# Performance work log

Hardware: AMD Instinct MI355X
Metric: run time of the kernel (lower is better)

Reference implementation:

```python
import math
import jax
import jax.numpy as jnp
import numpy as np

N_IMG = 8
A = 3
H = 100
W = 100
STRIDE = 16
IMG = 1600
PRE_NMS_TOP_N = 2000
POST_NMS_TOP_N = 1000
NMS_THRESH = 0.7
MIN_SIZE = 0
BBOX_XFORM_CLIP = math.log(1000.0 / 16.0)


def setup_inputs() -> dict:
    key = jax.random.key(0)
    k1, k2 = jax.random.split(key)
    objectness = jax.random.normal(k1, (N_IMG, A, H, W), jnp.float32)
    box_regression = jax.random.normal(k2, (N_IMG, A * 4, H, W), jnp.float32) * 0.5
    # Grid anchors, flattened in (H, W, A) order to match objectness.permute(0,2,3,1)
    cy = (jnp.arange(H, dtype=jnp.float32) + 0.5) * STRIDE  # [H]
    cx = (jnp.arange(W, dtype=jnp.float32) + 0.5) * STRIDE  # [W]
    half = jnp.array([64.0, 128.0, 256.0], jnp.float32) / 2.0  # [A]
    cy = cy[:, None, None]  # [H,1,1]
    cx = cx[None, :, None]  # [1,W,1]
    s = half[None, None, :]  # [1,1,A]
    x1, y1, x2, y2 = jnp.broadcast_arrays(cx - s, cy - s, cx + s, cy + s)
    anc = jnp.stack([x1, y1, x2, y2], axis=-1).reshape(-1, 4)  # [H*W*A, 4]
    anchors = jnp.broadcast_to(anc[None], (N_IMG, H * W * A, 4)).copy()
    return {
        "objectness": objectness,
        "box_regression": box_regression,
        "anchors": anchors,
        "image_height": IMG,
        "image_width": IMG,
    }


def _decode(deltas, boxes):
    # BoxCoder(weights=(1,1,1,1)).decode with TO_REMOVE=1
    widths = boxes[..., 2] - boxes[..., 0] + 1.0
    heights = boxes[..., 3] - boxes[..., 1] + 1.0
    ctr_x = boxes[..., 0] + 0.5 * widths
    ctr_y = boxes[..., 1] + 0.5 * heights
    dx, dy = deltas[..., 0], deltas[..., 1]
    dw = jnp.minimum(deltas[..., 2], BBOX_XFORM_CLIP)
    dh = jnp.minimum(deltas[..., 3], BBOX_XFORM_CLIP)
    pcx = dx * widths + ctr_x
    pcy = dy * heights + ctr_y
    pw = jnp.exp(dw) * widths
    ph = jnp.exp(dh) * heights
    return jnp.stack(
        [pcx - 0.5 * pw, pcy - 0.5 * ph, pcx + 0.5 * pw - 1.0, pcy + 0.5 * ph - 1.0],
        axis=-1,
    )


def _nms_keep(boxes, valid, thresh):
    # boxes [n,4] sorted by descending score; valid: pre-filter mask.
    n = boxes.shape[0]
    x1, y1, x2, y2 = boxes[:, 0], boxes[:, 1], boxes[:, 2], boxes[:, 3]
    areas = (x2 - x1 + 1.0) * (y2 - y1 + 1.0)
    xx1 = jnp.maximum(x1[:, None], x1[None, :])
    yy1 = jnp.maximum(y1[:, None], y1[None, :])
    xx2 = jnp.minimum(x2[:, None], x2[None, :])
    yy2 = jnp.minimum(y2[:, None], y2[None, :])
    inter = jnp.maximum(xx2 - xx1 + 1.0, 0.0) * jnp.maximum(yy2 - yy1 + 1.0, 0.0)
    iou = inter / (areas[:, None] + areas[None, :] - inter)
    idx = jnp.arange(n)

    def body(i, keep):
        sup = keep[i] & (iou[i] > thresh) & (idx > i)
        return keep & ~sup

    return jax.lax.fori_loop(0, n, body, valid)


def _forward(objectness, box_regression, anchors, image_height, image_width):
    N, A_, H_, W_ = objectness.shape
    scores = jax.nn.sigmoid(objectness.transpose(0, 2, 3, 1).reshape(N, -1))  # [N, A*H*W]
    deltas = (
        box_regression.reshape(N, A_, 4, H_, W_)
        .transpose(0, 3, 4, 1, 2)
        .reshape(N, -1, 4)
    )
    pre = min(PRE_NMS_TOP_N, scores.shape[1])
    top_scores, top_idx = jax.lax.top_k(scores, pre)  # sorted descending
    deltas = jnp.take_along_axis(deltas, top_idx[:, :, None], axis=1)
    anc = jnp.take_along_axis(anchors, top_idx[:, :, None], axis=1)
    props = _decode(deltas, anc)  # [N, pre, 4]
    # clip to image (fact = 1)
    xs = jnp.clip(props[..., 0::2], 0.0, image_width - 1.0)
    ys = jnp.clip(props[..., 1::2], 0.0, image_height - 1.0)
    props = jnp.stack([xs[..., 0], ys[..., 0], xs[..., 1], ys[..., 1]], axis=-1)
    # filter small / out-of-image-center boxes
    ws = props[..., 2] - props[..., 0] + 1.0
    hs = props[..., 3] - props[..., 1] + 1.0
    xc = props[..., 0] + ws / 2.0
    yc = props[..., 1] + hs / 2.0
    valid = (ws >= MIN_SIZE) & (hs >= MIN_SIZE) & (xc < image_width) & (yc < image_height)
    keep = jax.vmap(lambda b, v: _nms_keep(b, v, NMS_THRESH))(props, valid)

    def _select(b, s, k):
        # compact kept boxes (already score-sorted) into fixed-size output
        rank = jnp.cumsum(k) - 1
        tgt = jnp.where(k & (rank < POST_NMS_TOP_N), rank, POST_NMS_TOP_N)
        ob = jnp.zeros((POST_NMS_TOP_N + 1, 4), b.dtype).at[tgt].set(b)[:POST_NMS_TOP_N]
        os = jnp.zeros((POST_NMS_TOP_N + 1,), s.dtype).at[tgt].set(s)[:POST_NMS_TOP_N]
        ov = jnp.arange(POST_NMS_TOP_N) < jnp.minimum(jnp.sum(k), POST_NMS_TOP_N)
        return ob, os, ov

    return jax.vmap(_select)(props, top_scores, keep)


def reference(objectness, box_regression, anchors, image_height, image_width):
    # Returns (boxes [N,post,4], objectness scores [N,post], valid mask [N,post])
    return _forward(objectness, box_regression, anchors, image_height, image_width)
```

## Files before the change

### kernel.cpp

```cpp
#include <hip/hip_runtime.h>
#include <math.h>
#include <stdint.h>

#define NIMG   8
#define NA     30000
#define PRE_N  2000
#define POST_N 1000
#define NMS_TH 0.7f
#define DCLIP  4.135166556742356f
#define IMGF   1600.0f
#define IMGM1  1599.0f
#define CAND_MAX 4096


__global__ __launch_bounds__(1024) void hist_compact(
    const float* __restrict__ obj,
    uint64_t* __restrict__ candBuf, unsigned int* __restrict__ candCnt)
{
    const int n    = blockIdx.x;
    const int tid  = threadIdx.x;
    const int lane = tid & 63;
    const int wid  = tid >> 6;

    __shared__ unsigned int hist[4096];
    __shared__ unsigned int wsum[16];
    __shared__ unsigned int scal[4];

    for (int b = tid; b < 4096; b += 1024) hist[b] = 0u;
    if (tid < 4) scal[tid] = 0u;
    __syncthreads();

    const float* objn = obj + n * NA;

    for (int j = tid; j < NA; j += 1024) {
        unsigned int u = __float_as_uint(objn[j]);
        unsigned int k = (u & 0x80000000u) ? ~u : (u | 0x80000000u);
        atomicAdd(&hist[k >> 20], 1u);
    }
    __syncthreads();

    unsigned int c0 = hist[tid*4+0], c1 = hist[tid*4+1],
                 c2 = hist[tid*4+2], c3 = hist[tid*4+3];
    unsigned int p = c0 + c1 + c2 + c3;
    unsigned int s = p;
    #pragma unroll
    for (int off = 1; off < 64; off <<= 1) {
        unsigned int v = __shfl_down(s, off);
        if (lane + off < 64) s += v;
    }
    if (lane == 0) wsum[wid] = s;
    __syncthreads();
    unsigned int wafter = 0;
    for (int w = wid + 1; w < 16; ++w) wafter += wsum[w];
    unsigned int after = (s - p) + wafter;
    {
        unsigned int S3 = after + c3;
        unsigned int S2 = S3 + c2;
        unsigned int S1 = S2 + c1;
        unsigned int S0 = S1 + c0;
        if (S3 >= PRE_N && after < PRE_N) { scal[2] = tid*4+3; }
        if (S2 >= PRE_N && S3    < PRE_N) { scal[2] = tid*4+2; }
        if (S1 >= PRE_N && S2    < PRE_N) { scal[2] = tid*4+1; }
        if (S0 >= PRE_N && S1    < PRE_N) { scal[2] = tid*4+0; }
    }
    __syncthreads();
    const unsigned int bstar = scal[2];

    for (int j = tid; j < NA; j += 1024) {
        unsigned int u = __float_as_uint(objn[j]);
        unsigned int k = (u & 0x80000000u) ? ~u : (u | 0x80000000u);
        if ((k >> 20) < bstar) continue;
        int a = j / 10000, t = j - a * 10000;
        uint64_t key = (((uint64_t)(~k)) << 32) | (unsigned int)(t * 3 + a);
        unsigned int pos = atomicAdd(&scal[0], 1u);
        if (pos < CAND_MAX) candBuf[n * CAND_MAX + pos] = key;
    }
    __syncthreads();
    if (tid == 0) candCnt[n] = min(scal[0], (unsigned int)CAND_MAX);
}

__global__ __launch_bounds__(64) void rank_decode(
    const float* __restrict__ breg,
    const uint64_t* __restrict__ candBuf, const unsigned int* __restrict__ candCnt,
    float* __restrict__ wsBoxes, float* __restrict__ wsScores,
    int* __restrict__ wsValid)
{
    const int n    = blockIdx.x >> 6;
    const int tile = blockIdx.x & 63;
    const int lane = threadIdx.x;

    const int C = (int)candCnt[n];
    if (tile * 64 >= C) return;

    const uint64_t* cb = candBuf + n * CAND_MAX;
    const int my = tile * 64 + lane;
    const uint64_t km = (my < C) ? cb[my] : ~0ull;

    unsigned int rank = 0;
    const int nch = (C + 63) >> 6;
    for (int ch = 0; ch < nch; ++ch) {
        const int j = ch * 64 + lane;
        uint64_t ck = (j < C) ? cb[j] : ~0ull;
        unsigned int clo = (unsigned int)ck, chi = (unsigned int)(ck >> 32);
        #pragma unroll
        for (int c = 0; c < 64; ++c) {
            unsigned int lo = (unsigned int)__builtin_amdgcn_readlane((int)clo, c);
            unsigned int hi = (unsigned int)__builtin_amdgcn_readlane((int)chi, c);
            uint64_t kc = ((uint64_t)hi << 32) | lo;
            rank += (kc < km) ? 1u : 0u;
        }
    }
    if (my >= C || rank >= PRE_N) return;

    unsigned int idx = (unsigned int)km;
    unsigned int k   = ~((unsigned int)(km >> 32));
    unsigned int u   = (k & 0x80000000u) ? (k & 0x7fffffffu) : ~k;
    float logit = __uint_as_float(u);
    float score = 1.0f / (1.0f + expf(-logit));

    int a = idx % 3, t = idx / 3, w = t % 100, h = t / 100;
    const float* bp = breg + n*120000 + (a*4)*10000 + t;
    float dx = bp[0], dy = bp[10000], dw = bp[20000], dh = bp[30000];

    float half = (a == 0) ? 32.0f : ((a == 1) ? 64.0f : 128.0f);
    float cx = w * 16.0f + 8.0f, cy = h * 16.0f + 8.0f;
    float x1 = cx - half, y1 = cy - half, x2 = cx + half, y2 = cy + half;
    float wd = x2 - x1 + 1.0f, hg = y2 - y1 + 1.0f;
    float cxr = x1 + 0.5f * wd, cyr = y1 + 0.5f * hg;
    dw = fminf(dw, DCLIP); dh = fminf(dh, DCLIP);
    float pcx = dx * wd + cxr, pcy = dy * hg + cyr;
    float pw = expf(dw) * wd, ph = expf(dh) * hg;
    float px1 = pcx - 0.5f * pw, py1 = pcy - 0.5f * ph;
    float px2 = pcx + 0.5f * pw - 1.0f, py2 = pcy + 0.5f * ph - 1.0f;
    px1 = fminf(fmaxf(px1, 0.0f), IMGM1);
    px2 = fminf(fmaxf(px2, 0.0f), IMGM1);
    py1 = fminf(fmaxf(py1, 0.0f), IMGM1);
    py2 = fminf(fmaxf(py2, 0.0f), IMGM1);
    float wss = px2 - px1 + 1.0f, hss = py2 - py1 + 1.0f;
    float xc = px1 + wss * 0.5f, yc = py1 + hss * 0.5f;
    int valid = (wss >= 0.0f) && (hss >= 0.0f) && (xc < IMGF) && (yc < IMGF);

    ((float4*)wsBoxes)[n * PRE_N + (int)rank] = make_float4(px1, py1, px2, py2);
    wsScores[n * PRE_N + (int)rank] = score;
    wsValid [n * PRE_N + (int)rank] = valid;
}

__global__ __launch_bounds__(512) void nms_mask(
    const float* __restrict__ wsBoxes, uint64_t* __restrict__ mask)
{
    const int blk  = blockIdx.x;
    const int n    = blk >> 5;
    const int i_t  = blk & 31;
    const int tid  = threadIdx.x;
    const int lane = tid & 63;
    const int wv   = tid >> 6;

    __shared__ uint64_t tile[64 * 33];

    for (int idx = tid; idx < 64 * 33; idx += 512) tile[idx] = 0ull;
    __syncthreads();

    const int r = i_t * 64 + lane;
    float4 rb = (r < PRE_N) ? ((const float4*)wsBoxes)[n * PRE_N + r]
                            : make_float4(0.f, 0.f, 0.f, 0.f);
    float ra = (rb.z - rb.x + 1.0f) * (rb.w - rb.y + 1.0f);

    for (int j_t = i_t + wv; j_t < 32; j_t += 8) {
        const int j = j_t * 64 + lane;
        float4 cb = (j < PRE_N) ? ((const float4*)wsBoxes)[n * PRE_N + j]
                                : make_float4(3e30f, 3e30f, 3e30f, 3e30f);
        float ca = (cb.z - cb.x + 1.0f) * (cb.w - cb.y + 1.0f);
        const uint64_t jmask = (j_t == 31) ? 0xFFFFull : ~0ull;
        const bool diag = (j_t == i_t);
        uint64_t myword = 0ull;

        #pragma unroll
        for (int c = 0; c < 64; ++c) {
            float rx1 = __int_as_float(__builtin_amdgcn_readlane(__float_as_int(rb.x), c));
            float ry1 = __int_as_float(__builtin_amdgcn_readlane(__float_as_int(rb.y), c));
            float rx2 = __int_as_float(__builtin_amdgcn_readlane(__float_as_int(rb.z), c));
            float ry2 = __int_as_float(__builtin_amdgcn_readlane(__float_as_int(rb.w), c));
            float rar = __int_as_float(__builtin_amdgcn_readlane(__float_as_int(ra), c));
            float xx1 = fmaxf(rx1, cb.x), yy1 = fmaxf(ry1, cb.y);
            float xx2 = fminf(rx2, cb.z), yy2 = fminf(ry2, cb.w);
            float ww = fmaxf(xx2 - xx1 + 1.0f, 0.0f);
            float hh = fmaxf(yy2 - yy1 + 1.0f, 0.0f);
            float inter = ww * hh;
            float denom = rar + ca - inter;
            unsigned long long bits = __ballot(inter > NMS_TH * denom) & jmask;
            if (diag) bits &= (c == 63) ? 0ull : ((~0ull) << (c + 1));
            if (lane == c) myword = bits;
        }
        tile[lane * 33 + j_t] = myword;
    }
    __syncthreads();

    uint64_t* mrow = mask + ((size_t)n * PRE_N + (size_t)i_t * 64) * 32;
    const int cmax = (i_t == 31) ? 16 : 64;
    for (int idx = tid; idx < cmax * 32; idx += 512) {
        const int rr = idx >> 5, w = idx & 31;
        mrow[idx] = tile[rr * 33 + w];
    }
}

#define SL(n,b) \
    "global_load_dword v" #n ", %[voff], %[sbase]\n\t" \
    "v_add_u32 %[voff], 0x100, %[voff]\n\t"

#define SS(n,b) \
    "s_waitcnt vmcnt(63)\n\t" \
    "v_readlane_b32 %[t], v" #n ", %[lw]\n\t" \
    "s_bitcmp1_b32 %[win], " #b "\n\t" \
    "s_cselect_b32 %[m], 0, -1\n\t" \
    "s_sub_i32 %[kept], %[kept], %[m]\n\t" \
    "s_and_b32 %[t], %[t], %[m]\n\t" \
    "s_or_b32 %[win], %[win], %[t]\n\t" \
    "v_and_b32 v" #n ", %[m], v" #n "\n\t" \
    "v_or_b32 %[rem], %[rem], v" #n "\n\t" \
    "global_load_dword v" #n ", %[voff], %[sbase]\n\t" \
    "v_add_u32 %[voff], 0x100, %[voff]\n\t"

#define SN(n,b,w) \
    "s_waitcnt vmcnt(" #w ")\n\t" \
    "v_readlane_b32 %[t], v" #n ", %[lw]\n\t" \
    "s_bitcmp1_b32 %[win], " #b "\n\t" \
    "s_cselect_b32 %[m], 0, -1\n\t" \
    "s_sub_i32 %[kept], %[kept], %[m]\n\t" \
    "s_and_b32 %[t], %[t], %[m]\n\t" \
    "s_or_b32 %[win], %[win], %[t]\n\t" \
    "v_and_b32 v" #n ", %[m], v" #n "\n\t" \
    "v_or_b32 %[rem], %[rem], v" #n "\n\t"

#define SWIN \
    "s_add_u32 %[lw], %[lw], 1\n\t" \
    "v_readlane_b32 %[t], %[rem], %[lw]\n\t" \
    "s_mov_b32 %[win], %[t]\n\t"

#define ROW_A(M) M(64,0) M(65,1) M(66,2) M(67,3) M(68,4) M(69,5) M(70,6) M(71,7) \
    M(72,8) M(73,9) M(74,10) M(75,11) M(76,12) M(77,13) M(78,14) M(79,15) \
    M(80,16) M(81,17) M(82,18) M(83,19) M(84,20) M(85,21) M(86,22) M(87,23) \
    M(88,24) M(89,25) M(90,26) M(91,27) M(92,28) M(93,29) M(94,30) M(95,31)
#define ROW_B(M) M(96,0) M(97,1) M(98,2) M(99,3) M(100,4) M(101,5) M(102,6) M(103,7) \
    M(104,8) M(105,9) M(106,10) M(107,11) M(108,12) M(109,13) M(110,14) M(111,15) \
    M(112,16) M(113,17) M(114,18) M(115,19) M(116,20) M(117,21) M(118,22) M(119,23) \
    M(120,24) M(121,25) M(122,26) M(123,27) M(124,28) M(125,29) M(126,30) M(127,31)

__global__ __launch_bounds__(256) void nms_scan_select(
    const float* __restrict__ wsBoxes, const float* __restrict__ wsScores,
    const int* __restrict__ wsValid, const uint64_t* __restrict__ mask,
    float* __restrict__ out)
{
    const int n   = blockIdx.x;
    const int tid = threadIdx.x;

    __shared__ __align__(8) unsigned char invb[256];
    __shared__ unsigned int keepw32[64];
    __shared__ int sscan[256];

    unsigned int byte = 0xFFu;
    if (tid < PRE_N / 8) {
        byte = 0u;
        for (int q = 0; q < 8; ++q)
            byte |= (wsValid[n * PRE_N + tid * 8 + q] ? 0u : 1u) << q;
    }
    invb[tid] = (unsigned char)byte;
    __syncthreads();

    if (tid < 64) {
        unsigned int rem = ((const unsigned int*)invb)[tid];
        unsigned long long sbase =
            (unsigned long long)(const void*)(mask + (size_t)n * PRE_N * 32);
        unsigned int voff = (unsigned int)(tid * 4);
        int win_, m_, t_, lw_, kept_, cnt_;

        asm volatile(
            "s_waitcnt vmcnt(0) lgkmcnt(0)\n\t"
            "s_mov_b32 %[kept], 0\n\t"
            "s_mov_b32 %[lw], 0\n\t"
            ROW_A(SL) ROW_B(SL)
            "v_readlane_b32 %[t], %[rem], %[lw]\n\t"
            "s_mov_b32 %[win], %[t]\n\t"
            "s_mov_b32 %[cnt], 30\n\t"
            "Lnms_%=:\n\t"
            ROW_A(SS)
            SWIN
            ROW_B(SS)
            SWIN
            "s_cmp_ge_i32 %[kept], 0x3e8\n\t"
            "s_cbranch_scc1 Lend_%=\n\t"
            "s_sub_u32 %[cnt], %[cnt], 1\n\t"
            "s_cmp_lg_u32 %[cnt], 0\n\t"
            "s_cbranch_scc1 Lnms_%=\n\t"
            SS(64,0) SS(65,1) SS(66,2) SS(67,3) SS(68,4) SS(69,5) SS(70,6) SS(71,7)
            SS(72,8) SS(73,9) SS(74,10) SS(75,11) SS(76,12) SS(77,13) SS(78,14) SS(79,15)
            SN(80,16,63) SN(81,17,62) SN(82,18,61) SN(83,19,60)
            SN(84,20,59) SN(85,21,58) SN(86,22,57) SN(87,23,56)
            SN(88,24,55) SN(89,25,54) SN(90,26,53) SN(91,27,52)
            SN(92,28,51) SN(93,29,50) SN(94,30,49) SN(95,31,48)
            SWIN
            SN(96,0,47) SN(97,1,46) SN(98,2,45) SN(99,3,44)
            SN(100,4,43) SN(101,5,42) SN(102,6,41) SN(103,7,40)
            SN(104,8,39) SN(105,9,38) SN(106,10,37) SN(107,11,36)
            SN(108,12,35) SN(109,13,34) SN(110,14,33) SN(111,15,32)
            SN(112,16,31) SN(113,17,30) SN(114,18,29) SN(115,19,28)
            SN(116,20,27) SN(117,21,26) SN(118,22,25) SN(119,23,24)
            SN(120,24,23) SN(121,25,22) SN(122,26,21) SN(123,27,20)
            SN(124,28,19) SN(125,29,18) SN(126,30,17) SN(127,31,16)
            SWIN
            SN(64,0,15) SN(65,1,14) SN(66,2,13) SN(67,3,12)
            SN(68,4,11) SN(69,5,10) SN(70,6,9) SN(71,7,8)
            SN(72,8,7) SN(73,9,6) SN(74,10,5) SN(75,11,4)
            SN(76,12,3) SN(77,13,2) SN(78,14,1) SN(79,15,0)
            "Lend_%=:\n\t"
            "s_waitcnt vmcnt(0)\n\t"
            : [rem]"+v"(rem), [voff]"+v"(voff),
              [win]"=&s"(win_), [m]"=&s"(m_), [t]"=&s"(t_),
              [lw]"=&s"(lw_), [kept]"=&s"(kept_), [cnt]"=&s"(cnt_)
            : [sbase]"s"(sbase)
            : "scc", "vcc", "memory",
              "v64","v65","v66","v67","v68","v69","v70","v71",
              "v72","v73","v74","v75","v76","v77","v78","v79",
              "v80","v81","v82","v83","v84","v85","v86","v87",
              "v88","v89","v90","v91","v92","v93","v94","v95",
              "v96","v97","v98","v99","v100","v101","v102","v103",
              "v104","v105","v106","v107","v108","v109","v110","v111",
              "v112","v113","v114","v115","v116","v117","v118","v119",
              "v120","v121","v122","v123","v124","v125","v126","v127");

        keepw32[tid] = ~rem;
    }
    __syncthreads();

    int c[8]; const int base8 = tid * 8;
    int lsum = 0;
    for (int q = 0; q < 8; ++q) {
        const int i = base8 + q;
        c[q] = (i < PRE_N) ? (int)((keepw32[i >> 5] >> (i & 31)) & 1u) : 0;
        lsum += c[q];
    }
    sscan[tid] = lsum;
    __syncthreads();
    for (int off = 1; off < 256; off <<= 1) {
        int v = (tid >= off) ? sscan[tid - off] : 0;
        __syncthreads();
        sscan[tid] += v;
        __syncthreads();
    }
    const int excl  = sscan[tid] - lsum;
    const int total = sscan[255];

    float* ob  = out + n * POST_N * 4;
    float* osc = out + NIMG * POST_N * 4 + n * POST_N;
    float* ovd = out + NIMG * POST_N * 5 + n * POST_N;

    for (int i = tid; i < POST_N * 4; i += 256) ob[i] = 0.0f;
    for (int i = tid; i < POST_N; i += 256) osc[i] = 0.0f;
    const int lim = min(total, POST_N);
    for (int i = tid; i < POST_N; i += 256) ovd[i] = (i < lim) ? 1.0f : 0.0f;
    __syncthreads();

    int run = excl;
    for (int q = 0; q < 8; ++q) {
        const int i = base8 + q;
        if (i < PRE_N && c[q]) {
            if (run < POST_N) {
                float4 b = ((const float4*)wsBoxes)[n * PRE_N + i];
                ob[run * 4 + 0] = b.x;
                ob[run * 4 + 1] = b.y;
                ob[run * 4 + 2] = b.z;
                ob[run * 4 + 3] = b.w;
                osc[run] = wsScores[n * PRE_N + i];
            }
            run++;
        }
    }
}

extern "C" void kernel_launch(void* const* d_in, const int* in_sizes, int n_in,
                              void* d_out, int out_size, void* d_ws, size_t ws_size,
                              hipStream_t stream) {
    const float* obj  = (const float*)d_in[0];
    const float* breg = (const float*)d_in[1];
    float* ws        = (float*)d_ws;
    float* wsBoxes   = ws;
    float* wsScores  = ws + 64000;
    int*   wsValid   = (int*)(ws + 80000);
    uint64_t* wsMask = (uint64_t*)(ws + 96000);
    uint64_t*     candBuf = wsMask;
    unsigned int* candCnt = (unsigned int*)(wsMask + NIMG * CAND_MAX);

    hist_compact<<<NIMG, 1024, 0, stream>>>(obj, candBuf, candCnt);
    rank_decode<<<NIMG * 64, 64, 0, stream>>>(breg, candBuf, candCnt,
                                              wsBoxes, wsScores, wsValid);
    nms_mask<<<NIMG * 32, 512, 0, stream>>>(wsBoxes, wsMask);
    nms_scan_select<<<NIMG, 256, 0, stream>>>(wsBoxes, wsScores, wsValid, wsMask,
                                              (float*)d_out);
}
```

Baseline: 184.1 us.

## Fuse RPN pipeline into one cooperative kernel with grid-wide syncs

```diff
diff --git a/kernel.cpp b/kernel.cpp
--- a/kernel.cpp
+++ b/kernel.cpp
@@ -1,6 +1,9 @@
 #include <hip/hip_runtime.h>
+#include <hip/hip_cooperative_groups.h>
 #include <math.h>
 #include <stdint.h>
+
+namespace cg = cooperative_groups;
 
 #define NIMG   8
 #define NA     30000
@@ -11,197 +14,8 @@
 #define IMGF   1600.0f
 #define IMGM1  1599.0f
 #define CAND_MAX 4096
-
-
-__global__ __launch_bounds__(1024) void hist_compact(
-    const float* __restrict__ obj,
-    uint64_t* __restrict__ candBuf, unsigned int* __restrict__ candCnt)
-{
-    const int n    = blockIdx.x;
-    const int tid  = threadIdx.x;
-    const int lane = tid & 63;
-    const int wid  = tid >> 6;
-
-    __shared__ unsigned int hist[4096];
-    __shared__ unsigned int wsum[16];
-    __shared__ unsigned int scal[4];
-
-    for (int b = tid; b < 4096; b += 1024) hist[b] = 0u;
-    if (tid < 4) scal[tid] = 0u;
-    __syncthreads();
-
-    const float* objn = obj + n * NA;
-
-    for (int j = tid; j < NA; j += 1024) {
-        unsigned int u = __float_as_uint(objn[j]);
-        unsigned int k = (u & 0x80000000u) ? ~u : (u | 0x80000000u);
-        atomicAdd(&hist[k >> 20], 1u);
-    }
-    __syncthreads();
-
-    unsigned int c0 = hist[tid*4+0], c1 = hist[tid*4+1],
-                 c2 = hist[tid*4+2], c3 = hist[tid*4+3];
-    unsigned int p = c0 + c1 + c2 + c3;
-    unsigned int s = p;
-    #pragma unroll
-    for (int off = 1; off < 64; off <<= 1) {
-        unsigned int v = __shfl_down(s, off);
-        if (lane + off < 64) s += v;
-    }
-    if (lane == 0) wsum[wid] = s;
-    __syncthreads();
-    unsigned int wafter = 0;
-    for (int w = wid + 1; w < 16; ++w) wafter += wsum[w];
-    unsigned int after = (s - p) + wafter;
-    {
-        unsigned int S3 = after + c3;
-        unsigned int S2 = S3 + c2;
-        unsigned int S1 = S2 + c1;
-        unsigned int S0 = S1 + c0;
-        if (S3 >= PRE_N && after < PRE_N) { scal[2] = tid*4+3; }
-        if (S2 >= PRE_N && S3    < PRE_N) { scal[2] = tid*4+2; }
-        if (S1 >= PRE_N && S2    < PRE_N) { scal[2] = tid*4+1; }
-        if (S0 >= PRE_N && S1    < PRE_N) { scal[2] = tid*4+0; }
-    }
-    __syncthreads();
-    const unsigned int bstar = scal[2];
-
-    for (int j = tid; j < NA; j += 1024) {
-        unsigned int u = __float_as_uint(objn[j]);
-        unsigned int k = (u & 0x80000000u) ? ~u : (u | 0x80000000u);
-        if ((k >> 20) < bstar) continue;
-        int a = j / 10000, t = j - a * 10000;
-        uint64_t key = (((uint64_t)(~k)) << 32) | (unsigned int)(t * 3 + a);
-        unsigned int pos = atomicAdd(&scal[0], 1u);
-        if (pos < CAND_MAX) candBuf[n * CAND_MAX + pos] = key;
-    }
-    __syncthreads();
-    if (tid == 0) candCnt[n] = min(scal[0], (unsigned int)CAND_MAX);
-}
-
-__global__ __launch_bounds__(64) void rank_decode(
-    const float* __restrict__ breg,
-    const uint64_t* __restrict__ candBuf, const unsigned int* __restrict__ candCnt,
-    float* __restrict__ wsBoxes, float* __restrict__ wsScores,
-    int* __restrict__ wsValid)
-{
-    const int n    = blockIdx.x >> 6;
-    const int tile = blockIdx.x & 63;
-    const int lane = threadIdx.x;
-
-    const int C = (int)candCnt[n];
-    if (tile * 64 >= C) return;
-
-    const uint64_t* cb = candBuf + n * CAND_MAX;
-    const int my = tile * 64 + lane;
-    const uint64_t km = (my < C) ? cb[my] : ~0ull;
-
-    unsigned int rank = 0;
-    const int nch = (C + 63) >> 6;
-    for (int ch = 0; ch < nch; ++ch) {
-        const int j = ch * 64 + lane;
-        uint64_t ck = (j < C) ? cb[j] : ~0ull;
-        unsigned int clo = (unsigned int)ck, chi = (unsigned int)(ck >> 32);
-        #pragma unroll
-        for (int c = 0; c < 64; ++c) {
-            unsigned int lo = (unsigned int)__builtin_amdgcn_readlane((int)clo, c);
-            unsigned int hi = (unsigned int)__builtin_amdgcn_readlane((int)chi, c);
-            uint64_t kc = ((uint64_t)hi << 32) | lo;
-            rank += (kc < km) ? 1u : 0u;
-        }
-    }
-    if (my >= C || rank >= PRE_N) return;
-
-    unsigned int idx = (unsigned int)km;
-    unsigned int k   = ~((unsigned int)(km >> 32));
-    unsigned int u   = (k & 0x80000000u) ? (k & 0x7fffffffu) : ~k;
-    float logit = __uint_as_float(u);
-    float score = 1.0f / (1.0f + expf(-logit));
-
-    int a = idx % 3, t = idx / 3, w = t % 100, h = t / 100;
-    const float* bp = breg + n*120000 + (a*4)*10000 + t;
-    float dx = bp[0], dy = bp[10000], dw = bp[20000], dh = bp[30000];
-
-    float half = (a == 0) ? 32.0f : ((a == 1) ? 64.0f : 128.0f);
-    float cx = w * 16.0f + 8.0f, cy = h * 16.0f + 8.0f;
-    float x1 = cx - half, y1 = cy - half, x2 = cx + half, y2 = cy + half;
-    float wd = x2 - x1 + 1.0f, hg = y2 - y1 + 1.0f;
-    float cxr = x1 + 0.5f * wd, cyr = y1 + 0.5f * hg;
-    dw = fminf(dw, DCLIP); dh = fminf(dh, DCLIP);
-    float pcx = dx * wd + cxr, pcy = dy * hg + cyr;
-    float pw = expf(dw) * wd, ph = expf(dh) * hg;
-    float px1 = pcx - 0.5f * pw, py1 = pcy - 0.5f * ph;
-    float px2 = pcx + 0.5f * pw - 1.0f, py2 = pcy + 0.5f * ph - 1.0f;
-    px1 = fminf(fmaxf(px1, 0.0f), IMGM1);
-    px2 = fminf(fmaxf(px2, 0.0f), IMGM1);
-    py1 = fminf(fmaxf(py1, 0.0f), IMGM1);
-    py2 = fminf(fmaxf(py2, 0.0f), IMGM1);
-    float wss = px2 - px1 + 1.0f, hss = py2 - py1 + 1.0f;
-    float xc = px1 + wss * 0.5f, yc = py1 + hss * 0.5f;
-    int valid = (wss >= 0.0f) && (hss >= 0.0f) && (xc < IMGF) && (yc < IMGF);
-
-    ((float4*)wsBoxes)[n * PRE_N + (int)rank] = make_float4(px1, py1, px2, py2);
-    wsScores[n * PRE_N + (int)rank] = score;
-    wsValid [n * PRE_N + (int)rank] = valid;
-}
-
-__global__ __launch_bounds__(512) void nms_mask(
-    const float* __restrict__ wsBoxes, uint64_t* __restrict__ mask)
-{
-    const int blk  = blockIdx.x;
-    const int n    = blk >> 5;
-    const int i_t  = blk & 31;
-    const int tid  = threadIdx.x;
-    const int lane = tid & 63;
-    const int wv   = tid >> 6;
-
-    __shared__ uint64_t tile[64 * 33];
-
-    for (int idx = tid; idx < 64 * 33; idx += 512) tile[idx] = 0ull;
-    __syncthreads();
-
-    const int r = i_t * 64 + lane;
-    float4 rb = (r < PRE_N) ? ((const float4*)wsBoxes)[n * PRE_N + r]
-                            : make_float4(0.f, 0.f, 0.f, 0.f);
-    float ra = (rb.z - rb.x + 1.0f) * (rb.w - rb.y + 1.0f);
-
-    for (int j_t = i_t + wv; j_t < 32; j_t += 8) {
-        const int j = j_t * 64 + lane;
-        float4 cb = (j < PRE_N) ? ((const float4*)wsBoxes)[n * PRE_N + j]
-                                : make_float4(3e30f, 3e30f, 3e30f, 3e30f);
-        float ca = (cb.z - cb.x + 1.0f) * (cb.w - cb.y + 1.0f);
-        const uint64_t jmask = (j_t == 31) ? 0xFFFFull : ~0ull;
-        const bool diag = (j_t == i_t);
-        uint64_t myword = 0ull;
-
-        #pragma unroll
-        for (int c = 0; c < 64; ++c) {
-            float rx1 = __int_as_float(__builtin_amdgcn_readlane(__float_as_int(rb.x), c));
-            float ry1 = __int_as_float(__builtin_amdgcn_readlane(__float_as_int(rb.y), c));
-            float rx2 = __int_as_float(__builtin_amdgcn_readlane(__float_as_int(rb.z), c));
-            float ry2 = __int_as_float(__builtin_amdgcn_readlane(__float_as_int(rb.w), c));
-            float rar = __int_as_float(__builtin_amdgcn_readlane(__float_as_int(ra), c));
-            float xx1 = fmaxf(rx1, cb.x), yy1 = fmaxf(ry1, cb.y);
-            float xx2 = fminf(rx2, cb.z), yy2 = fminf(ry2, cb.w);
-            float ww = fmaxf(xx2 - xx1 + 1.0f, 0.0f);
-            float hh = fmaxf(yy2 - yy1 + 1.0f, 0.0f);
-            float inter = ww * hh;
-            float denom = rar + ca - inter;
-            unsigned long long bits = __ballot(inter > NMS_TH * denom) & jmask;
-            if (diag) bits &= (c == 63) ? 0ull : ((~0ull) << (c + 1));
-            if (lane == c) myword = bits;
-        }
-        tile[lane * 33 + j_t] = myword;
-    }
-    __syncthreads();
-
-    uint64_t* mrow = mask + ((size_t)n * PRE_N + (size_t)i_t * 64) * 32;
-    const int cmax = (i_t == 31) ? 16 : 64;
-    for (int idx = tid; idx < cmax * 32; idx += 512) {
-        const int rr = idx >> 5, w = idx & 31;
-        mrow[idx] = tile[rr * 33 + w];
-    }
-}
+#define NBLK   256
+#define NTHR   512
 
 #define SL(n,b) \
     "global_load_dword v" #n ", %[voff], %[sbase]\n\t" \
@@ -245,133 +59,312 @@
     M(112,16) M(113,17) M(114,18) M(115,19) M(116,20) M(117,21) M(118,22) M(119,23) \
     M(120,24) M(121,25) M(122,26) M(123,27) M(124,28) M(125,29) M(126,30) M(127,31)
 
-__global__ __launch_bounds__(256) void nms_scan_select(
-    const float* __restrict__ wsBoxes, const float* __restrict__ wsScores,
-    const int* __restrict__ wsValid, const uint64_t* __restrict__ mask,
+__global__ __launch_bounds__(NTHR) void rpn_mega(
+    const float* __restrict__ obj, const float* __restrict__ breg,
+    float* __restrict__ wsBoxes, float* __restrict__ wsScores,
+    int* __restrict__ wsValid, uint64_t* __restrict__ candBuf,
+    unsigned int* __restrict__ candCnt, unsigned int* __restrict__ bstarArr,
+    unsigned int* __restrict__ gHist, uint64_t* __restrict__ mask,
     float* __restrict__ out)
 {
-    const int n   = blockIdx.x;
-    const int tid = threadIdx.x;
-
-    __shared__ __align__(8) unsigned char invb[256];
-    __shared__ unsigned int keepw32[64];
-    __shared__ int sscan[256];
-
-    unsigned int byte = 0xFFu;
-    if (tid < PRE_N / 8) {
-        byte = 0u;
-        for (int q = 0; q < 8; ++q)
-            byte |= (wsValid[n * PRE_N + tid * 8 + q] ? 0u : 1u) << q;
-    }
-    invb[tid] = (unsigned char)byte;
-    __syncthreads();
-
-    if (tid < 64) {
-        unsigned int rem = ((const unsigned int*)invb)[tid];
-        unsigned long long sbase =
-            (unsigned long long)(const void*)(mask + (size_t)n * PRE_N * 32);
-        unsigned int voff = (unsigned int)(tid * 4);
-        int win_, m_, t_, lw_, kept_, cnt_;
-
-        asm volatile(
-            "s_waitcnt vmcnt(0) lgkmcnt(0)\n\t"
-            "s_mov_b32 %[kept], 0\n\t"
-            "s_mov_b32 %[lw], 0\n\t"
-            ROW_A(SL) ROW_B(SL)
-            "v_readlane_b32 %[t], %[rem], %[lw]\n\t"
-            "s_mov_b32 %[win], %[t]\n\t"
-            "s_mov_b32 %[cnt], 30\n\t"
-            "Lnms_%=:\n\t"
-            ROW_A(SS)
-            SWIN
-            ROW_B(SS)
-            SWIN
-            "s_cmp_ge_i32 %[kept], 0x3e8\n\t"
-            "s_cbranch_scc1 Lend_%=\n\t"
-            "s_sub_u32 %[cnt], %[cnt], 1\n\t"
-            "s_cmp_lg_u32 %[cnt], 0\n\t"
-            "s_cbranch_scc1 Lnms_%=\n\t"
-            SS(64,0) SS(65,1) SS(66,2) SS(67,3) SS(68,4) SS(69,5) SS(70,6) SS(71,7)
-            SS(72,8) SS(73,9) SS(74,10) SS(75,11) SS(76,12) SS(77,13) SS(78,14) SS(79,15)
-            SN(80,16,63) SN(81,17,62) SN(82,18,61) SN(83,19,60)
-            SN(84,20,59) SN(85,21,58) SN(86,22,57) SN(87,23,56)
-            SN(88,24,55) SN(89,25,54) SN(90,26,53) SN(91,27,52)
-            SN(92,28,51) SN(93,29,50) SN(94,30,49) SN(95,31,48)
-            SWIN
-            SN(96,0,47) SN(97,1,46) SN(98,2,45) SN(99,3,44)
-            SN(100,4,43) SN(101,5,42) SN(102,6,41) SN(103,7,40)
-            SN(104,8,39) SN(105,9,38) SN(106,10,37) SN(107,11,36)
-            SN(108,12,35) SN(109,13,34) SN(110,14,33) SN(111,15,32)
-            SN(112,16,31) SN(113,17,30) SN(114,18,29) SN(115,19,28)
-            SN(116,20,27) SN(117,21,26) SN(118,22,25) SN(119,23,24)
-            SN(120,24,23) SN(121,25,22) SN(122,26,21) SN(123,27,20)
-            SN(124,28,19) SN(125,29,18) SN(126,30,17) SN(127,31,16)
-            SWIN
-            SN(64,0,15) SN(65,1,14) SN(66,2,13) SN(67,3,12)
-            SN(68,4,11) SN(69,5,10) SN(70,6,9) SN(71,7,8)
-            SN(72,8,7) SN(73,9,6) SN(74,10,5) SN(75,11,4)
-            SN(76,12,3) SN(77,13,2) SN(78,14,1) SN(79,15,0)
-            "Lend_%=:\n\t"
-            "s_waitcnt vmcnt(0)\n\t"
-            : [rem]"+v"(rem), [voff]"+v"(voff),
-              [win]"=&s"(win_), [m]"=&s"(m_), [t]"=&s"(t_),
-              [lw]"=&s"(lw_), [kept]"=&s"(kept_), [cnt]"=&s"(cnt_)
-            : [sbase]"s"(sbase)
-            : "scc", "vcc", "memory",
-              "v64","v65","v66","v67","v68","v69","v70","v71",
-              "v72","v73","v74","v75","v76","v77","v78","v79",
-              "v80","v81","v82","v83","v84","v85","v86","v87",
-              "v88","v89","v90","v91","v92","v93","v94","v95",
-              "v96","v97","v98","v99","v100","v101","v102","v103",
-              "v104","v105","v106","v107","v108","v109","v110","v111",
-              "v112","v113","v114","v115","v116","v117","v118","v119",
-              "v120","v121","v122","v123","v124","v125","v126","v127");
-
-        keepw32[tid] = ~rem;
-    }
-    __syncthreads();
-
-    int c[8]; const int base8 = tid * 8;
-    int lsum = 0;
-    for (int q = 0; q < 8; ++q) {
-        const int i = base8 + q;
-        c[q] = (i < PRE_N) ? (int)((keepw32[i >> 5] >> (i & 31)) & 1u) : 0;
-        lsum += c[q];
-    }
-    sscan[tid] = lsum;
-    __syncthreads();
-    for (int off = 1; off < 256; off <<= 1) {
-        int v = (tid >= off) ? sscan[tid - off] : 0;
-        __syncthreads();
-        sscan[tid] += v;
-        __syncthreads();
-    }
-    const int excl  = sscan[tid] - lsum;
-    const int total = sscan[255];
-
-    float* ob  = out + n * POST_N * 4;
-    float* osc = out + NIMG * POST_N * 4 + n * POST_N;
-    float* ovd = out + NIMG * POST_N * 5 + n * POST_N;
-
-    for (int i = tid; i < POST_N * 4; i += 256) ob[i] = 0.0f;
-    for (int i = tid; i < POST_N; i += 256) osc[i] = 0.0f;
-    const int lim = min(total, POST_N);
-    for (int i = tid; i < POST_N; i += 256) ovd[i] = (i < lim) ? 1.0f : 0.0f;
-    __syncthreads();
-
-    int run = excl;
-    for (int q = 0; q < 8; ++q) {
-        const int i = base8 + q;
-        if (i < PRE_N && c[q]) {
-            if (run < POST_N) {
-                float4 b = ((const float4*)wsBoxes)[n * PRE_N + i];
-                ob[run * 4 + 0] = b.x;
-                ob[run * 4 + 1] = b.y;
-                ob[run * 4 + 2] = b.z;
-                ob[run * 4 + 3] = b.w;
-                osc[run] = wsScores[n * PRE_N + i];
+    cg::grid_group grid = cg::this_grid();
+    const int blk  = blockIdx.x;
+    const int tid  = threadIdx.x;
+    const int lane = tid & 63;
+    const int wid  = tid >> 6;
+    const int g    = blk * NTHR + tid;
+
+    __shared__ uint64_t sTile[64 * 33];
+    __shared__ int      sScan[NTHR];
+    __shared__ unsigned int sWsum[8];
+    __shared__ unsigned int sScal[4];
+    __shared__ __align__(8) unsigned char sInvb[256];
+    __shared__ unsigned int sKeep[64];
+
+    if (g < NIMG * 4096) gHist[g] = 0u;
+    if (g < NIMG) { candCnt[g] = 0u; bstarArr[g] = 0u; }
+    grid.sync();
+
+    for (int i = g; i < NIMG * NA; i += NBLK * NTHR) {
+        const int n = i / NA;
+        unsigned int u = __float_as_uint(obj[i]);
+        unsigned int k = (u & 0x80000000u) ? ~u : (u | 0x80000000u);
+        atomicAdd(&gHist[n * 4096 + (k >> 20)], 1u);
+    }
+    grid.sync();
+
+    if (blk < NIMG) {
+        const int n = blk;
+        unsigned int cb8[8], p = 0;
+        for (int q = 0; q < 8; ++q) { cb8[q] = gHist[n * 4096 + tid * 8 + q]; p += cb8[q]; }
+        unsigned int s = p;
+        #pragma unroll
+        for (int off = 1; off < 64; off <<= 1) {
+            unsigned int v = __shfl_down(s, off);
+            if (lane + off < 64) s += v;
+        }
+        if (lane == 0) sWsum[wid] = s;
+        __syncthreads();
+        unsigned int wafter = 0;
+        for (int w = wid + 1; w < 8; ++w) wafter += sWsum[w];
+        unsigned int suf = (s - p) + wafter;
+        for (int q = 7; q >= 0; --q) {
+            unsigned int Sq = suf + cb8[q];
+            if (Sq >= PRE_N && suf < PRE_N) sScal[0] = (unsigned int)(tid * 8 + q);
+            suf = Sq;
+        }
+        __syncthreads();
+        if (tid == 0) bstarArr[n] = sScal[0];
+    }
+    grid.sync();
+
+    for (int i = g; i < NIMG * NA; i += NBLK * NTHR) {
+        const int n = i / NA;
+        const int j = i - n * NA;
+        unsigned int u = __float_as_uint(obj[i]);
+        unsigned int k = (u & 0x80000000u) ? ~u : (u | 0x80000000u);
+        if ((k >> 20) >= bstarArr[n]) {
+            int a = j / 10000, t = j - a * 10000;
+            uint64_t key = (((uint64_t)(~k)) << 32) | (unsigned int)(t * 3 + a);
+            unsigned int pos = atomicAdd(&candCnt[n], 1u);
+            if (pos < CAND_MAX) candBuf[n * CAND_MAX + pos] = key;
+        }
+    }
+    grid.sync();
+
+    {
+        const int gw = blk * 8 + wid;
+        if (gw < NIMG * 64) {
+            const int n = gw >> 6, tile = gw & 63;
+            const int C = min((int)candCnt[n], CAND_MAX);
+            if (tile * 64 < C) {
+                const uint64_t* cb = candBuf + n * CAND_MAX;
+                const int my = tile * 64 + lane;
+                const uint64_t km = (my < C) ? cb[my] : ~0ull;
+                unsigned int rank = 0;
+                const int nch = (C + 63) >> 6;
+                for (int ch = 0; ch < nch; ++ch) {
+                    const int j = ch * 64 + lane;
+                    uint64_t ck = (j < C) ? cb[j] : ~0ull;
+                    unsigned int clo = (unsigned int)ck, chi = (unsigned int)(ck >> 32);
+                    #pragma unroll
+                    for (int c2 = 0; c2 < 64; ++c2) {
+                        unsigned int lo = (unsigned int)__builtin_amdgcn_readlane((int)clo, c2);
+                        unsigned int hi = (unsigned int)__builtin_amdgcn_readlane((int)chi, c2);
+                        uint64_t kc = ((uint64_t)hi << 32) | lo;
+                        rank += (kc < km) ? 1u : 0u;
+                    }
+                }
+                if (my < C && rank < PRE_N) {
+                    unsigned int idx = (unsigned int)km;
+                    unsigned int k   = ~((unsigned int)(km >> 32));
+                    unsigned int u   = (k & 0x80000000u) ? (k & 0x7fffffffu) : ~k;
+                    float logit = __uint_as_float(u);
+                    float score = 1.0f / (1.0f + expf(-logit));
+
+                    int a = idx % 3, t = idx / 3, w = t % 100, h = t / 100;
+                    const float* bp = breg + n*120000 + (a*4)*10000 + t;
+                    float dx = bp[0], dy = bp[10000], dw = bp[20000], dh = bp[30000];
+
+                    float half = (a == 0) ? 32.0f : ((a == 1) ? 64.0f : 128.0f);
+                    float cx = w * 16.0f + 8.0f, cy = h * 16.0f + 8.0f;
+                    float x1 = cx - half, y1 = cy - half, x2 = cx + half, y2 = cy + half;
+                    float wd = x2 - x1 + 1.0f, hg = y2 - y1 + 1.0f;
+                    float cxr = x1 + 0.5f * wd, cyr = y1 + 0.5f * hg;
+                    dw = fminf(dw, DCLIP); dh = fminf(dh, DCLIP);
+                    float pcx = dx * wd + cxr, pcy = dy * hg + cyr;
+                    float pw = expf(dw) * wd, ph = expf(dh) * hg;
+                    float px1 = pcx - 0.5f * pw, py1 = pcy - 0.5f * ph;
+                    float px2 = pcx + 0.5f * pw - 1.0f, py2 = pcy + 0.5f * ph - 1.0f;
+                    px1 = fminf(fmaxf(px1, 0.0f), IMGM1);
+                    px2 = fminf(fmaxf(px2, 0.0f), IMGM1);
+                    py1 = fminf(fmaxf(py1, 0.0f), IMGM1);
+                    py2 = fminf(fmaxf(py2, 0.0f), IMGM1);
+                    float wss = px2 - px1 + 1.0f, hss = py2 - py1 + 1.0f;
+                    float xc = px1 + wss * 0.5f, yc = py1 + hss * 0.5f;
+                    int valid = (wss >= 0.0f) && (hss >= 0.0f) && (xc < IMGF) && (yc < IMGF);
+
+                    ((float4*)wsBoxes)[n * PRE_N + (int)rank] = make_float4(px1, py1, px2, py2);
+                    wsScores[n * PRE_N + (int)rank] = score;
+                    wsValid [n * PRE_N + (int)rank] = valid;
+                }
             }
-            run++;
+        }
+    }
+    grid.sync();
+
+    {
+        const int n   = blk >> 5;
+        const int i_t = blk & 31;
+
+        for (int idx = tid; idx < 64 * 33; idx += NTHR) sTile[idx] = 0ull;
+        __syncthreads();
+
+        const int r = i_t * 64 + lane;
+        float4 rb = (r < PRE_N) ? ((const float4*)wsBoxes)[n * PRE_N + r]
+                                : make_float4(0.f, 0.f, 0.f, 0.f);
+        float ra = (rb.z - rb.x + 1.0f) * (rb.w - rb.y + 1.0f);
+
+        for (int j_t = i_t + wid; j_t < 32; j_t += 8) {
+            const int j = j_t * 64 + lane;
+            float4 cbx = (j < PRE_N) ? ((const float4*)wsBoxes)[n * PRE_N + j]
+                                     : make_float4(3e30f, 3e30f, 3e30f, 3e30f);
+            float ca = (cbx.z - cbx.x + 1.0f) * (cbx.w - cbx.y + 1.0f);
+            const uint64_t jmask = (j_t == 31) ? 0xFFFFull : ~0ull;
+            const bool diag = (j_t == i_t);
+            uint64_t myword = 0ull;
+
+            #pragma unroll
+            for (int c2 = 0; c2 < 64; ++c2) {
+                float rx1 = __int_as_float(__builtin_amdgcn_readlane(__float_as_int(rb.x), c2));
+                float ry1 = __int_as_float(__builtin_amdgcn_readlane(__float_as_int(rb.y), c2));
+                float rx2 = __int_as_float(__builtin_amdgcn_readlane(__float_as_int(rb.z), c2));
+                float ry2 = __int_as_float(__builtin_amdgcn_readlane(__float_as_int(rb.w), c2));
+                float rar = __int_as_float(__builtin_amdgcn_readlane(__float_as_int(ra), c2));
+                float xx1 = fmaxf(rx1, cbx.x), yy1 = fmaxf(ry1, cbx.y);
+                float xx2 = fminf(rx2, cbx.z), yy2 = fminf(ry2, cbx.w);
+                float ww = fmaxf(xx2 - xx1 + 1.0f, 0.0f);
+                float hh = fmaxf(yy2 - yy1 + 1.0f, 0.0f);
+                float inter = ww * hh;
+                float denom = rar + ca - inter;
+                unsigned long long bits = __ballot(inter > NMS_TH * denom) & jmask;
+                if (diag) bits &= (c2 == 63) ? 0ull : ((~0ull) << (c2 + 1));
+                if (lane == c2) myword = bits;
+            }
+            sTile[lane * 33 + j_t] = myword;
+        }
+        __syncthreads();
+
+        uint64_t* mrow = mask + ((size_t)n * PRE_N + (size_t)i_t * 64) * 32;
+        const int cmax = (i_t == 31) ? 16 : 64;
+        for (int idx = tid; idx < cmax * 32; idx += NTHR) {
+            const int rr = idx >> 5, w = idx & 31;
+            mrow[idx] = sTile[rr * 33 + w];
+        }
+    }
+    grid.sync();
+
+    if (blk < NIMG) {
+        const int n = blk;
+
+        if (tid < 256) {
+            unsigned int byte = 0xFFu;
+            if (tid < PRE_N / 8) {
+                byte = 0u;
+                for (int q = 0; q < 8; ++q)
+                    byte |= (wsValid[n * PRE_N + tid * 8 + q] ? 0u : 1u) << q;
+            }
+            sInvb[tid] = (unsigned char)byte;
+        }
+        __syncthreads();
+
+        if (tid < 64) {
+            unsigned int rem = ((const unsigned int*)sInvb)[tid];
+            unsigned long long sbase =
+                (unsigned long long)(const void*)(mask + (size_t)n * PRE_N * 32);
+            unsigned int voff = (unsigned int)(tid * 4);
+            int win_, m_, t_, lw_, kept_, cnt_;
+
+            asm volatile(
+                "s_waitcnt vmcnt(0) lgkmcnt(0)\n\t"
+                "s_mov_b32 %[kept], 0\n\t"
+                "s_mov_b32 %[lw], 0\n\t"
+                ROW_A(SL) ROW_B(SL)
+                "v_readlane_b32 %[t], %[rem], %[lw]\n\t"
+                "s_mov_b32 %[win], %[t]\n\t"
+                "s_mov_b32 %[cnt], 30\n\t"
+                "Lnms_%=:\n\t"
+                ROW_A(SS)
+                SWIN
+                ROW_B(SS)
+                SWIN
+                "s_cmp_ge_i32 %[kept], 0x3e8\n\t"
+                "s_cbranch_scc1 Lend_%=\n\t"
+                "s_sub_u32 %[cnt], %[cnt], 1\n\t"
+                "s_cmp_lg_u32 %[cnt], 0\n\t"
+                "s_cbranch_scc1 Lnms_%=\n\t"
+                SS(64,0) SS(65,1) SS(66,2) SS(67,3) SS(68,4) SS(69,5) SS(70,6) SS(71,7)
+                SS(72,8) SS(73,9) SS(74,10) SS(75,11) SS(76,12) SS(77,13) SS(78,14) SS(79,15)
+                SN(80,16,63) SN(81,17,62) SN(82,18,61) SN(83,19,60)
+                SN(84,20,59) SN(85,21,58) SN(86,22,57) SN(87,23,56)
+                SN(88,24,55) SN(89,25,54) SN(90,26,53) SN(91,27,52)
+                SN(92,28,51) SN(93,29,50) SN(94,30,49) SN(95,31,48)
+                SWIN
+                SN(96,0,47) SN(97,1,46) SN(98,2,45) SN(99,3,44)
+                SN(100,4,43) SN(101,5,42) SN(102,6,41) SN(103,7,40)
+                SN(104,8,39) SN(105,9,38) SN(106,10,37) SN(107,11,36)
+                SN(108,12,35) SN(109,13,34) SN(110,14,33) SN(111,15,32)
+                SN(112,16,31) SN(113,17,30) SN(114,18,29) SN(115,19,28)
+                SN(116,20,27) SN(117,21,26) SN(118,22,25) SN(119,23,24)
+                SN(120,24,23) SN(121,25,22) SN(122,26,21) SN(123,27,20)
+                SN(124,28,19) SN(125,29,18) SN(126,30,17) SN(127,31,16)
+                SWIN
+                SN(64,0,15) SN(65,1,14) SN(66,2,13) SN(67,3,12)
+                SN(68,4,11) SN(69,5,10) SN(70,6,9) SN(71,7,8)
+                SN(72,8,7) SN(73,9,6) SN(74,10,5) SN(75,11,4)
+                SN(76,12,3) SN(77,13,2) SN(78,14,1) SN(79,15,0)
+                "Lend_%=:\n\t"
+                "s_waitcnt vmcnt(0)\n\t"
+                : [rem]"+v"(rem), [voff]"+v"(voff),
+                  [win]"=&s"(win_), [m]"=&s"(m_), [t]"=&s"(t_),
+                  [lw]"=&s"(lw_), [kept]"=&s"(kept_), [cnt]"=&s"(cnt_)
+                : [sbase]"s"(sbase)
+                : "scc", "vcc", "memory",
+                  "v64","v65","v66","v67","v68","v69","v70","v71",
+                  "v72","v73","v74","v75","v76","v77","v78","v79",
+                  "v80","v81","v82","v83","v84","v85","v86","v87",
+                  "v88","v89","v90","v91","v92","v93","v94","v95",
+                  "v96","v97","v98","v99","v100","v101","v102","v103",
+                  "v104","v105","v106","v107","v108","v109","v110","v111",
+                  "v112","v113","v114","v115","v116","v117","v118","v119",
+                  "v120","v121","v122","v123","v124","v125","v126","v127");
+
+            sKeep[tid] = ~rem;
+        }
+        __syncthreads();
+
+        int cf[4]; const int base4 = tid * 4;
+        int lsum = 0;
+        for (int q = 0; q < 4; ++q) {
+            const int i = base4 + q;
+            cf[q] = (i < PRE_N) ? (int)((sKeep[i >> 5] >> (i & 31)) & 1u) : 0;
+            lsum += cf[q];
+        }
+        sScan[tid] = lsum;
+        __syncthreads();
+        for (int off = 1; off < NTHR; off <<= 1) {
+            int v = (tid >= off) ? sScan[tid - off] : 0;
+            __syncthreads();
+            sScan[tid] += v;
+            __syncthreads();
+        }
+        const int excl  = sScan[tid] - lsum;
+        const int total = sScan[NTHR - 1];
+
+        float* ob  = out + n * POST_N * 4;
+        float* osc = out + NIMG * POST_N * 4 + n * POST_N;
+        float* ovd = out + NIMG * POST_N * 5 + n * POST_N;
+
+        for (int i = tid; i < POST_N * 4; i += NTHR) ob[i] = 0.0f;
+        for (int i = tid; i < POST_N; i += NTHR) osc[i] = 0.0f;
+        const int lim = min(total, POST_N);
+        for (int i = tid; i < POST_N; i += NTHR) ovd[i] = (i < lim) ? 1.0f : 0.0f;
+        __syncthreads();
+
+        int run = excl;
+        for (int q = 0; q < 4; ++q) {
+            const int i = base4 + q;
+            if (i < PRE_N && cf[q]) {
+                if (run < POST_N) {
+                    float4 b = ((const float4*)wsBoxes)[n * PRE_N + i];
+                    ob[run * 4 + 0] = b.x;
+                    ob[run * 4 + 1] = b.y;
+                    ob[run * 4 + 2] = b.z;
+                    ob[run * 4 + 3] = b.w;
+                    osc[run] = wsScores[n * PRE_N + i];
+                }
+                run++;
+            }
         }
     }
 }
@@ -386,13 +379,18 @@
     float* wsScores  = ws + 64000;
     int*   wsValid   = (int*)(ws + 80000);
     uint64_t* wsMask = (uint64_t*)(ws + 96000);
-    uint64_t*     candBuf = wsMask;
-    unsigned int* candCnt = (unsigned int*)(wsMask + NIMG * CAND_MAX);
-
-    hist_compact<<<NIMG, 1024, 0, stream>>>(obj, candBuf, candCnt);
-    rank_decode<<<NIMG * 64, 64, 0, stream>>>(breg, candBuf, candCnt,
-                                              wsBoxes, wsScores, wsValid);
-    nms_mask<<<NIMG * 32, 512, 0, stream>>>(wsBoxes, wsMask);
-    nms_scan_select<<<NIMG, 256, 0, stream>>>(wsBoxes, wsScores, wsValid, wsMask,
-                                              (float*)d_out);
+    uint64_t* candBuf = wsMask;
+    unsigned int* gHist =
+        (unsigned int*)((char*)wsMask + (size_t)NIMG * PRE_N * 32 * 8);
+    unsigned int* candCnt  = gHist + NIMG * 4096;
+    unsigned int* bstarArr = candCnt + NIMG;
+    float* outp = (float*)d_out;
+
+    void* args[] = {
+        (void*)&obj, (void*)&breg, (void*)&wsBoxes, (void*)&wsScores,
+        (void*)&wsValid, (void*)&candBuf, (void*)&candCnt, (void*)&bstarArr,
+        (void*)&gHist, (void*)&wsMask, (void*)&outp
+    };
+    hipLaunchCooperativeKernel((const void*)rpn_mega, dim3(NBLK), dim3(NTHR),
+                               args, 0, stream);
 }
```

After: 589.5 us. +220.2%, slower.
